# Optimization experiments

Measured on AMD Instinct MI355X. Metric: run time of the kernel, lower is better.

The kernel has to match this reference:

```python
import jax, jax.numpy as jnp
import numpy as np

N_ITEMS = 7000
N_USERS = 30000
N_NODES = N_ITEMS + N_USERS  # 37000
D = 128        # embed_dim == user_embed_dim
E = 400000     # num edges
R = 10         # n_relation (num ratings)
NB = 8         # num_bases
B = 512        # batch of conversations
L = 100        # max context items per sample


def setup_inputs() -> dict:
    key = jax.random.key(0)
    ks = jax.random.split(key, 16)
    # edges: item (source) -> user (target), disjoint id ranges as in load_data
    src = jax.random.randint(ks[0], (E,), 0, N_ITEMS)
    dst = jax.random.randint(ks[1], (E,), N_ITEMS, N_NODES)
    edge_index = jnp.stack([src, dst]).astype(jnp.int64)
    edge_type = jax.random.randint(ks[2], (E,), 0, R).astype(jnp.int64)

    def make_ctx(k1, k2):
        c = jax.random.randint(k1, (B, L), 0, N_ITEMS)
        drop = jax.random.uniform(k2, (B, L)) < 0.3  # -1 padding as in batch lists
        return jnp.where(drop, -1, c).astype(jnp.int64)

    ctx_init = make_ctx(ks[3], ks[4])
    ctx_resp = make_ctx(ks[5], ks[6])

    s = 0.02
    basis = jax.random.normal(ks[7], (NB, N_NODES, D), jnp.float32) * s
    comp = jax.random.normal(ks[8], (R, NB), jnp.float32) * s
    root = jax.random.normal(ks[9], (N_NODES, D), jnp.float32) * s
    bias = jnp.zeros((D,), jnp.float32)
    attn_a = jax.random.normal(ks[10], (D, D), jnp.float32) * s
    attn_b = jax.random.normal(ks[11], (D,), jnp.float32) * s
    fc1_w = jax.random.normal(ks[12], (D, D), jnp.float32) * s
    fc1_b = jnp.zeros((D,), jnp.float32)
    fc2_w = jax.random.normal(ks[13], (D, D), jnp.float32) * s
    fc2_b = jnp.zeros((D,), jnp.float32)
    efc1_w = jax.random.normal(ks[14], (2 * D, D), jnp.float32) * s
    efc1_b = jnp.zeros((D,), jnp.float32)
    efc2_w = jax.random.normal(ks[15], (D, D), jnp.float32) * s
    efc2_b = jnp.zeros((D,), jnp.float32)
    return dict(edge_index=edge_index, edge_type=edge_type, ctx_init=ctx_init,
                ctx_resp=ctx_resp, basis=basis, comp=comp, root=root, bias=bias,
                attn_a=attn_a, attn_b=attn_b, fc1_w=fc1_w, fc1_b=fc1_b,
                fc2_w=fc2_w, fc2_b=fc2_b, efc1_w=efc1_w, efc1_b=efc1_b,
                efc2_w=efc2_w, efc2_b=efc2_b)


def _rgcn(basis, comp, root, bias, edge_index, edge_type):
    # RGCNConv with x=None: per-edge message W_{r_e}[src_e], mean-aggregated
    # per (target, relation), summed over relations, plus root lookup + bias.
    src, dst = edge_index[0], edge_index[1]
    nb, n, d = basis.shape
    r = comp.shape[0]
    cpe = comp[edge_type]  # [E, NB]
    msg = jnp.zeros((src.shape[0], d), basis.dtype)
    for b in range(nb):  # small fixed basis count; avoids [E,NB,D] gather
        msg = msg + cpe[:, b:b + 1] * basis[b][src]
    seg = dst * r + edge_type  # per-(node, relation) segment for mean aggr
    sums = jax.ops.segment_sum(msg, seg, num_segments=n * r).reshape(n, r, d)
    cnt = jax.ops.segment_sum(jnp.ones_like(edge_type, basis.dtype), seg,
                              num_segments=n * r).reshape(n, r, 1)
    return root + bias + (sums / jnp.maximum(cnt, 1.0)).sum(axis=1)  # [N, D]


def _item_user_means(node_emb, edge_index):
    # mean over users connected to each item (edge_idx[1][edge_idx[0]==item])
    src, dst = edge_index[0], edge_index[1]
    isum = jax.ops.segment_sum(node_emb[dst], src, num_segments=N_ITEMS)
    icnt = jax.ops.segment_sum(jnp.ones_like(src, node_emb.dtype), src,
                               num_segments=N_ITEMS)
    item_mean = isum / jnp.maximum(icnt, 1.0)[:, None]  # [N_ITEMS, D]
    return item_mean, icnt > 0


def _attn_pool(ctx, item_mean, item_has_users, attn_a, attn_b):
    # SelfAttentionBatch over each sample's item reps (padding/-1 & degree-0
    # items masked out; all-empty samples -> zeros, as in original).
    valid = ctx >= 0
    idx = jnp.clip(ctx, 0, N_ITEMS - 1)
    h = item_mean[idx]                       # [B, L, D]
    valid = valid & item_has_users[idx]
    e = jnp.einsum('bld,d->bl', jnp.tanh(jnp.einsum('bld,de->ble', h, attn_a)),
                   attn_b)
    attn = jax.nn.softmax(jnp.where(valid, e, -1e9), axis=-1)
    attn = jnp.where(valid, attn, 0.0)
    return jnp.einsum('bl,bld->bd', attn, h)  # [B, D]


def _project(x, w1, b1, w2, b2):
    # fc1 -> relu -> fc2 -> relu (as in _project_user_interaction_*)
    return jax.nn.relu(jax.nn.relu(x @ w1 + b1) @ w2 + b2)


def reference(edge_index, edge_type, ctx_init, ctx_resp, basis, comp, root,
              bias, attn_a, attn_b, fc1_w, fc1_b, fc2_w, fc2_b, efc1_w,
              efc1_b, efc2_w, efc2_b):
    node_emb = _rgcn(basis, comp, root, bias, edge_index, edge_type)
    item_mean, item_has = _item_user_means(node_emb, edge_index)
    p_init = _project(_attn_pool(ctx_init, item_mean, item_has, attn_a, attn_b),
                      fc1_w, fc1_b, fc2_w, fc2_b)
    p_resp = _project(_attn_pool(ctx_resp, item_mean, item_has, attn_a, attn_b),
                      fc1_w, fc1_b, fc2_w, fc2_b)
    both = jnp.concatenate([p_init, p_resp], axis=1)  # [B, 2D]
    profile = _project(both, efc1_w, efc1_b, efc2_w, efc2_b)  # [B, D]
    return profile, p_init, p_resp
```

## Files before the change

kernel.cpp:

```cpp
#include <hip/hip_runtime.h>
#include <math.h>

typedef unsigned int uint;

#define N_ITEMS 7000
#define N_NODES 37000
#define N_USERS 30000
#define DIM     128
#define HD      64
#define NREL    10
#define NBASES  8
#define BATCH   512
#define CTXL    100
#define E_MAX   400000

#define UCAP    64
#define ICAP    128

#define OFF_CNT    0
#define OFF_ICNT   (OFF_CNT + N_USERS * NREL)
#define OFF_UCNT   (OFF_ICNT + N_ITEMS)
#define ZERO_ELEMS (OFF_UCNT + N_USERS)
#define OFF_ICSR   ZERO_ELEMS
#define OFF_UCSR   (OFF_ICSR + N_ITEMS * ICAP)
#define OFF_WC     (OFF_UCSR + N_USERS * UCAP)
#define OFF_ACC    (OFF_WC + NREL * N_ITEMS * HD)
#define OFF_MEAN   (OFF_ACC + N_USERS * HD)
#define OFF_SCORE  (OFF_MEAN + N_ITEMS * HD)

__device__ __forceinline__ float2 bf2f(uint p) {
  float2 r;
  r.x = __uint_as_float(p << 16);
  r.y = __uint_as_float(p & 0xffff0000u);
  return r;
}
__device__ __forceinline__ uint f2bf(float x, float y) {
  uint a = __float_as_uint(x), b = __float_as_uint(y);
  a += 0x7fffu + ((a >> 16) & 1u);
  b += 0x7fffu + ((b >> 16) & 1u);
  return (a >> 16) | (b & 0xffff0000u);
}

__device__ __forceinline__ float wave_sum(float v) {
#pragma unroll
  for (int o = 1; o < 64; o <<= 1) v += __shfl_xor(v, o, 64);
  return v;
}
__device__ __forceinline__ float wave_max(float v) {
#pragma unroll
  for (int o = 1; o < 64; o <<= 1) v = fmaxf(v, __shfl_xor(v, o, 64));
  return v;
}

#define COMBINE_BLOCKS (N_ITEMS / 4)
__global__ __launch_bounds__(256) void k_initfill(const float* __restrict__ basis,
                                                  const float* __restrict__ comp,
                                                  uint* __restrict__ Wc,
                                                  const int* __restrict__ ei,
                                                  const int* __restrict__ et, int E,
                                                  int* __restrict__ cnt,
                                                  int* __restrict__ icnt,
                                                  int* __restrict__ ucnt,
                                                  int* __restrict__ icsr,
                                                  int* __restrict__ ucsr) {
  int tid = threadIdx.x;
  if (blockIdx.x < COMBINE_BLOCKS) {
    int i = blockIdx.x * 4 + (tid >> 6);
    int lane = tid & 63;
    float2 bb[NBASES];
#pragma unroll
    for (int b = 0; b < NBASES; ++b)
      bb[b] = ((const float2*)basis)[((size_t)b * N_NODES + i) * HD + lane];
#pragma unroll
    for (int r = 0; r < NREL; ++r) {
      float sx = 0.f, sy = 0.f;
#pragma unroll
      for (int b = 0; b < NBASES; ++b) {
        float c = comp[r * NBASES + b];
        sx = fmaf(c, bb[b].x, sx);
        sy = fmaf(c, bb[b].y, sy);
      }
      Wc[((size_t)i * NREL + r) * HD + lane] = f2bf(sx, sy);
    }
  } else {
    int e = (blockIdx.x - COMBINE_BLOCKS) * 256 + tid;
    if (e < E) {
      int s  = ei[e];
      int u0 = ei[E + e] - N_ITEMS;
      int t  = et[e];
      atomicAdd(&cnt[u0 * NREL + t], 1);
      int si = atomicAdd(&icnt[s], 1);
      if (si < ICAP) icsr[s * ICAP + si] = u0;
      int su = atomicAdd(&ucnt[u0], 1);
      if (su < UCAP) ucsr[u0 * UCAP + su] = s | (t << 16);
    }
  }
}

__global__ __launch_bounds__(256) void k_useragg(const int* __restrict__ ucnt,
                                                 const int* __restrict__ ucsr,
                                                 const int* __restrict__ cnt,
                                                 const uint* __restrict__ Wc,
                                                 const float* __restrict__ root,
                                                 uint* __restrict__ acc) {
  int tid = threadIdx.x;
  int u = blockIdx.x * 4 + (tid >> 6);
  int lane = tid & 63;
  int deg = ucnt[u];
  if (deg > UCAP) deg = UCAP;
  int base = u * UCAP;
  float wl = 0.f;
  if (lane < NREL) {
    int c = cnt[u * NREL + lane];
    wl = (c > 0) ? 1.0f / (float)c : 0.0f;
  }
  float2 av[8];
#pragma unroll
  for (int k = 0; k < 8; ++k) { av[k].x = 0.f; av[k].y = 0.f; }
  for (int j0 = 0; j0 < deg; j0 += 64) {
    int m = deg - j0;
    if (m > 64) m = 64;
    int pl = (lane < m) ? ucsr[base + j0 + lane] : 0;
    for (int kk = 0; kk < m; kk += 16) {
#pragma unroll
      for (int k = 0; k < 16; ++k) {
        int idx = kk + k;
        int p = __shfl(pl, idx & 63);
        int r = p >> 16;
        float w = (idx < m) ? __shfl(wl, r) : 0.f;
        uint q = Wc[((size_t)(p & 0xffff) * NREL + r) * HD + lane];
        float2 f = bf2f(q);
        av[k & 7].x = fmaf(w, f.x, av[k & 7].x);
        av[k & 7].y = fmaf(w, f.y, av[k & 7].y);
      }
    }
  }
  float2 rt = ((const float2*)root)[(size_t)(N_ITEMS + u) * HD + lane];
  rt.x += ((av[0].x + av[1].x) + (av[2].x + av[3].x)) +
          ((av[4].x + av[5].x) + (av[6].x + av[7].x));
  rt.y += ((av[0].y + av[1].y) + (av[2].y + av[3].y)) +
          ((av[4].y + av[5].y) + (av[6].y + av[7].y));
  acc[(size_t)u * HD + lane] = f2bf(rt.x, rt.y);
}

__global__ __launch_bounds__(256) void k_itemagg(const int* __restrict__ icnt,
                                                 const int* __restrict__ icsr,
                                                 const uint* __restrict__ acc,
                                                 const float* __restrict__ bias,
                                                 const float* __restrict__ attn_a,
                                                 const float* __restrict__ attn_b,
                                                 uint* __restrict__ mean,
                                                 float* __restrict__ score) {
  int tid = threadIdx.x;
  int i = blockIdx.x * 4 + (tid >> 6);
  int lane = tid & 63;
  int deg = icnt[i];
  int degc = (deg > ICAP) ? ICAP : deg;
  int base = i * ICAP;
  float2 av[8];
#pragma unroll
  for (int k = 0; k < 8; ++k) { av[k].x = 0.f; av[k].y = 0.f; }
  for (int j0 = 0; j0 < degc; j0 += 64) {
    int m = degc - j0;
    if (m > 64) m = 64;
    int pl = (lane < m) ? icsr[base + j0 + lane] : 0;
    for (int kk = 0; kk < m; kk += 16) {
#pragma unroll
      for (int k = 0; k < 16; ++k) {
        int idx = kk + k;
        int u0 = __shfl(pl, idx & 63);
        uint q = acc[(size_t)u0 * HD + lane];
        float2 f = bf2f(q);
        if (idx < m) {
          av[k & 7].x += f.x;
          av[k & 7].y += f.y;
        }
      }
    }
  }
  float sx = ((av[0].x + av[1].x) + (av[2].x + av[3].x)) +
             ((av[4].x + av[5].x) + (av[6].x + av[7].x));
  float sy = ((av[0].y + av[1].y) + (av[2].y + av[3].y)) +
             ((av[4].y + av[5].y) + (av[6].y + av[7].y));
  float2 mv = {0.f, 0.f};
  if (deg > 0) {
    float inv = 1.0f / (float)deg;
    float2 bv = ((const float2*)bias)[lane];
    mv.x = sx * inv + bv.x;
    mv.y = sy * inv + bv.y;
  }
  mean[(size_t)i * HD + lane] = f2bf(mv.x, mv.y);

  float z0 = 0.f, z1 = 0.f;
#pragma unroll 8
  for (int k2 = 0; k2 < HD; ++k2) {
    float hx = __shfl(mv.x, k2);
    float hy = __shfl(mv.y, k2);
    float2 w0 = ((const float2*)attn_a)[(size_t)(2 * k2) * HD + lane];
    float2 w1 = ((const float2*)attn_a)[(size_t)(2 * k2 + 1) * HD + lane];
    z0 = fmaf(hx, w0.x, z0); z1 = fmaf(hx, w0.y, z1);
    z0 = fmaf(hy, w1.x, z0); z1 = fmaf(hy, w1.y, z1);
  }
  float2 ab = ((const float2*)attn_b)[lane];
  float v = wave_sum(tanhf(z0) * ab.x + tanhf(z1) * ab.y);
  if (lane == 0) score[i] = (deg > 0) ? v : -1e9f;
}

__global__ __launch_bounds__(128) void k_batch2(const int* __restrict__ ctx0,
                                                const int* __restrict__ ctx1,
                                                const uint* __restrict__ mean,
                                                const float* __restrict__ score,
                                                const float* __restrict__ fc1_w,
                                                const float* __restrict__ fc1_b,
                                                const float* __restrict__ fc2_w,
                                                const float* __restrict__ fc2_b,
                                                const float* __restrict__ efc1_w,
                                                const float* __restrict__ efc1_b,
                                                const float* __restrict__ efc2_w,
                                                const float* __restrict__ efc2_b,
                                                float* __restrict__ out) {
  __shared__ float2 shp[2][HD];
  int b = blockIdx.x;
  int wv = threadIdx.x >> 6;
  int lane = threadIdx.x & 63;
  float2* out2 = (float2*)out;

  const int* cx = (wv ? ctx1 : ctx0) + (size_t)b * CTXL;
  int id0 = cx[lane];
  float e0 = (id0 >= 0) ? score[id0] : -1e9f;
  int id1 = -1;
  float e1 = -3.0e38f;
  if (lane < CTXL - 64) {
    id1 = cx[64 + lane];
    e1 = (id1 >= 0) ? score[id1] : -1e9f;
  }
  float mx = wave_max(fmaxf(e0, e1));
  float x0 = expf(e0 - mx);
  float x1 = (lane < CTXL - 64) ? expf(e1 - mx) : 0.f;
  float inv = 1.0f / wave_sum(x0 + x1);
  float w0 = (id0 >= 0) ? x0 * inv : 0.f;
  float w1 = (id1 >= 0) ? x1 * inv : 0.f;
  int i0 = (id0 >= 0) ? id0 : 0;
  int i1 = (id1 >= 0) ? id1 : 0;

  float2 av[4];
#pragma unroll
  for (int k = 0; k < 4; ++k) { av[k].x = 0.f; av[k].y = 0.f; }
  for (int j = 0; j < 64; j += 4) {
#pragma unroll
    for (int k = 0; k < 4; ++k) {
      int ii = __shfl(i0, j + k);
      float ww = __shfl(w0, j + k);
      float2 f = bf2f(mean[(size_t)ii * HD + lane]);
      av[k].x = fmaf(ww, f.x, av[k].x);
      av[k].y = fmaf(ww, f.y, av[k].y);
    }
  }
  for (int j = 0; j < CTXL - 64; j += 4) {
#pragma unroll
    for (int k = 0; k < 4; ++k) {
      int ii = __shfl(i1, j + k);
      float ww = __shfl(w1, j + k);
      float2 f = bf2f(mean[(size_t)ii * HD + lane]);
      av[k].x = fmaf(ww, f.x, av[k].x);
      av[k].y = fmaf(ww, f.y, av[k].y);
    }
  }
  float2 pool;
  pool.x = (av[0].x + av[1].x) + (av[2].x + av[3].x);
  pool.y = (av[0].y + av[1].y) + (av[2].y + av[3].y);

  float2 z = ((const float2*)fc1_b)[lane];
#pragma unroll 8
  for (int k2 = 0; k2 < HD; ++k2) {
    float hx = __shfl(pool.x, k2);
    float hy = __shfl(pool.y, k2);
    float2 wa = ((const float2*)fc1_w)[(size_t)(2 * k2) * HD + lane];
    float2 wb = ((const float2*)fc1_w)[(size_t)(2 * k2 + 1) * HD + lane];
    z.x = fmaf(hx, wa.x, z.x); z.y = fmaf(hx, wa.y, z.y);
    z.x = fmaf(hy, wb.x, z.x); z.y = fmaf(hy, wb.y, z.y);
  }
  z.x = fmaxf(z.x, 0.f);
  z.y = fmaxf(z.y, 0.f);

  float2 z2 = ((const float2*)fc2_b)[lane];
#pragma unroll 8
  for (int k2 = 0; k2 < HD; ++k2) {
    float hx = __shfl(z.x, k2);
    float hy = __shfl(z.y, k2);
    float2 wa = ((const float2*)fc2_w)[(size_t)(2 * k2) * HD + lane];
    float2 wb = ((const float2*)fc2_w)[(size_t)(2 * k2 + 1) * HD + lane];
    z2.x = fmaf(hx, wa.x, z2.x); z2.y = fmaf(hx, wa.y, z2.y);
    z2.x = fmaf(hy, wb.x, z2.x); z2.y = fmaf(hy, wb.y, z2.y);
  }
  z2.x = fmaxf(z2.x, 0.f);
  z2.y = fmaxf(z2.y, 0.f);
  out2[((size_t)(1 + wv) * BATCH + b) * HD + lane] = z2;
  shp[wv][lane] = z2;
  __syncthreads();

  if (wv == 0) {
    float2 p0 = shp[0][lane];
    float2 p1 = shp[1][lane];
    float2 zz = ((const float2*)efc1_b)[lane];
#pragma unroll 8
    for (int k2 = 0; k2 < HD; ++k2) {
      float hx = __shfl(p0.x, k2);
      float hy = __shfl(p0.y, k2);
      float2 wa = ((const float2*)efc1_w)[(size_t)(2 * k2) * HD + lane];
      float2 wb = ((const float2*)efc1_w)[(size_t)(2 * k2 + 1) * HD + lane];
      zz.x = fmaf(hx, wa.x, zz.x); zz.y = fmaf(hx, wa.y, zz.y);
      zz.x = fmaf(hy, wb.x, zz.x); zz.y = fmaf(hy, wb.y, zz.y);
    }
#pragma unroll 8
    for (int k2 = 0; k2 < HD; ++k2) {
      float hx = __shfl(p1.x, k2);
      float hy = __shfl(p1.y, k2);
      float2 wa = ((const float2*)efc1_w)[(size_t)(DIM + 2 * k2) * HD + lane];
      float2 wb = ((const float2*)efc1_w)[(size_t)(DIM + 2 * k2 + 1) * HD + lane];
      zz.x = fmaf(hx, wa.x, zz.x); zz.y = fmaf(hx, wa.y, zz.y);
      zz.x = fmaf(hy, wb.x, zz.x); zz.y = fmaf(hy, wb.y, zz.y);
    }
    zz.x = fmaxf(zz.x, 0.f);
    zz.y = fmaxf(zz.y, 0.f);

    float2 zf = ((const float2*)efc2_b)[lane];
#pragma unroll 8
    for (int k2 = 0; k2 < HD; ++k2) {
      float hx = __shfl(zz.x, k2);
      float hy = __shfl(zz.y, k2);
      float2 wa = ((const float2*)efc2_w)[(size_t)(2 * k2) * HD + lane];
      float2 wb = ((const float2*)efc2_w)[(size_t)(2 * k2 + 1) * HD + lane];
      zf.x = fmaf(hx, wa.x, zf.x); zf.y = fmaf(hx, wa.y, zf.y);
      zf.x = fmaf(hy, wb.x, zf.x); zf.y = fmaf(hy, wb.y, zf.y);
    }
    zf.x = fmaxf(zf.x, 0.f);
    zf.y = fmaxf(zf.y, 0.f);
    out2[(size_t)b * HD + lane] = zf;
  }
}

extern "C" void kernel_launch(void* const* d_in, const int* in_sizes, int n_in,
                              void* d_out, int out_size, void* d_ws, size_t ws_size,
                              hipStream_t stream) {
  const int*   ei     = (const int*)d_in[0];
  const int*   et     = (const int*)d_in[1];
  const int*   ctx0   = (const int*)d_in[2];
  const int*   ctx1   = (const int*)d_in[3];
  const float* basis  = (const float*)d_in[4];
  const float* comp   = (const float*)d_in[5];
  const float* root   = (const float*)d_in[6];
  const float* bias   = (const float*)d_in[7];
  const float* attn_a = (const float*)d_in[8];
  const float* attn_b = (const float*)d_in[9];
  const float* fc1_w  = (const float*)d_in[10];
  const float* fc1_b  = (const float*)d_in[11];
  const float* fc2_w  = (const float*)d_in[12];
  const float* fc2_b  = (const float*)d_in[13];
  const float* efc1_w = (const float*)d_in[14];
  const float* efc1_b = (const float*)d_in[15];
  const float* efc2_w = (const float*)d_in[16];
  const float* efc2_b = (const float*)d_in[17];
  float* out = (float*)d_out;

  const int E = in_sizes[1];

  float* ws   = (float*)d_ws;
  int*  cnt   = (int*)(ws + OFF_CNT);
  int*  icnt  = (int*)(ws + OFF_ICNT);
  int*  ucnt  = (int*)(ws + OFF_UCNT);
  int*  icsr  = (int*)(ws + OFF_ICSR);
  int*  ucsr  = (int*)(ws + OFF_UCSR);
  uint* Wc    = (uint*)(ws + OFF_WC);
  uint* acc   = (uint*)(ws + OFF_ACC);
  uint* mean  = (uint*)(ws + OFF_MEAN);
  float* score = ws + OFF_SCORE;

  hipMemsetAsync(d_ws, 0, (size_t)ZERO_ELEMS * sizeof(float), stream);

  int countBlocks = (E + 255) / 256;
  k_initfill<<<COMBINE_BLOCKS + countBlocks, 256, 0, stream>>>(
      basis, comp, Wc, ei, et, E, cnt, icnt, ucnt, icsr, ucsr);
  k_useragg<<<N_USERS / 4, 256, 0, stream>>>(ucnt, ucsr, cnt, Wc, root, acc);
  k_itemagg<<<N_ITEMS / 4, 256, 0, stream>>>(icnt, icsr, acc, bias, attn_a,
                                             attn_b, mean, score);
  k_batch2<<<BATCH, 128, 0, stream>>>(ctx0, ctx1, mean, score, fc1_w, fc1_b,
                                      fc2_w, fc2_b, efc1_w, efc1_b, efc2_w,
                                      efc2_b, out);
}
```

Before: 394.9 us.

## Process two nodes per wave and batch gathers before accumulating

Each wave in the user and item aggregation kernels now handles two nodes instead of one. It issues 32 independent row gathers into register arrays before doing any accumulation, so more loads are in flight at once and gather latency is hidden better. Both kernels gain a launch-bounds minimum-occupancy hint, and the grids are halved to match. The cost is higher register pressure and wasted work whenever the two paired nodes have unequal degrees, since the loop runs to the larger degree.

Measured after the change: 387.4 us, median of 2. No clear change (-1.9%).

```diff
diff --git a/kernel.cpp b/kernel.cpp
--- a/kernel.cpp
+++ b/kernel.cpp
@@ -97,113 +97,178 @@
   }
 }
 
-__global__ __launch_bounds__(256) void k_useragg(const int* __restrict__ ucnt,
-                                                 const int* __restrict__ ucsr,
-                                                 const int* __restrict__ cnt,
-                                                 const uint* __restrict__ Wc,
-                                                 const float* __restrict__ root,
-                                                 uint* __restrict__ acc) {
+__global__ __launch_bounds__(256, 4) void k_useragg(const int* __restrict__ ucnt,
+                                                    const int* __restrict__ ucsr,
+                                                    const int* __restrict__ cnt,
+                                                    const uint* __restrict__ Wc,
+                                                    const float* __restrict__ root,
+                                                    uint* __restrict__ acc) {
   int tid = threadIdx.x;
-  int u = blockIdx.x * 4 + (tid >> 6);
-  int lane = tid & 63;
-  int deg = ucnt[u];
-  if (deg > UCAP) deg = UCAP;
-  int base = u * UCAP;
-  float wl = 0.f;
+  int wid = tid >> 6, lane = tid & 63;
+  int uA = blockIdx.x * 8 + wid * 2;
+  int uB = uA + 1;
+  int degA = ucnt[uA]; if (degA > UCAP) degA = UCAP;
+  int degB = ucnt[uB]; if (degB > UCAP) degB = UCAP;
+  float wlA = 0.f, wlB = 0.f;
   if (lane < NREL) {
-    int c = cnt[u * NREL + lane];
-    wl = (c > 0) ? 1.0f / (float)c : 0.0f;
-  }
-  float2 av[8];
-#pragma unroll
-  for (int k = 0; k < 8; ++k) { av[k].x = 0.f; av[k].y = 0.f; }
-  for (int j0 = 0; j0 < deg; j0 += 64) {
-    int m = deg - j0;
-    if (m > 64) m = 64;
-    int pl = (lane < m) ? ucsr[base + j0 + lane] : 0;
-    for (int kk = 0; kk < m; kk += 16) {
-#pragma unroll
-      for (int k = 0; k < 16; ++k) {
-        int idx = kk + k;
-        int p = __shfl(pl, idx & 63);
-        int r = p >> 16;
-        float w = (idx < m) ? __shfl(wl, r) : 0.f;
-        uint q = Wc[((size_t)(p & 0xffff) * NREL + r) * HD + lane];
-        float2 f = bf2f(q);
-        av[k & 7].x = fmaf(w, f.x, av[k & 7].x);
-        av[k & 7].y = fmaf(w, f.y, av[k & 7].y);
-      }
-    }
-  }
-  float2 rt = ((const float2*)root)[(size_t)(N_ITEMS + u) * HD + lane];
-  rt.x += ((av[0].x + av[1].x) + (av[2].x + av[3].x)) +
-          ((av[4].x + av[5].x) + (av[6].x + av[7].x));
-  rt.y += ((av[0].y + av[1].y) + (av[2].y + av[3].y)) +
-          ((av[4].y + av[5].y) + (av[6].y + av[7].y));
-  acc[(size_t)u * HD + lane] = f2bf(rt.x, rt.y);
-}
-
-__global__ __launch_bounds__(256) void k_itemagg(const int* __restrict__ icnt,
-                                                 const int* __restrict__ icsr,
-                                                 const uint* __restrict__ acc,
-                                                 const float* __restrict__ bias,
-                                                 const float* __restrict__ attn_a,
-                                                 const float* __restrict__ attn_b,
-                                                 uint* __restrict__ mean,
-                                                 float* __restrict__ score) {
+    int cA = cnt[uA * NREL + lane];
+    int cB = cnt[uB * NREL + lane];
+    wlA = (cA > 0) ? 1.0f / (float)cA : 0.0f;
+    wlB = (cB > 0) ? 1.0f / (float)cB : 0.0f;
+  }
+  int plA = ucsr[uA * UCAP + lane];
+  int plB = ucsr[uB * UCAP + lane];
+
+  float2 avA[4], avB[4];
+#pragma unroll
+  for (int k = 0; k < 4; ++k) {
+    avA[k].x = 0.f; avA[k].y = 0.f;
+    avB[k].x = 0.f; avB[k].y = 0.f;
+  }
+  int mmax = (degA > degB) ? degA : degB;
+#pragma unroll 1
+  for (int kk = 0; kk < mmax; kk += 16) {
+    uint qA[16], qB[16];
+#pragma unroll
+    for (int k = 0; k < 16; ++k) {
+      int idx = kk + k;
+      int p = (idx < degA) ? __shfl(plA, idx & 63) : 0;
+      qA[k] = Wc[((size_t)(p & 0xffff) * NREL + (p >> 16)) * HD + lane];
+    }
+#pragma unroll
+    for (int k = 0; k < 16; ++k) {
+      int idx = kk + k;
+      int p = (idx < degB) ? __shfl(plB, idx & 63) : 0;
+      qB[k] = Wc[((size_t)(p & 0xffff) * NREL + (p >> 16)) * HD + lane];
+    }
+#pragma unroll
+    for (int k = 0; k < 16; ++k) {
+      int idx = kk + k;
+      int p = __shfl(plA, idx & 63);
+      float w = (idx < degA) ? __shfl(wlA, p >> 16) : 0.f;
+      float2 f = bf2f(qA[k]);
+      avA[k & 3].x = fmaf(w, f.x, avA[k & 3].x);
+      avA[k & 3].y = fmaf(w, f.y, avA[k & 3].y);
+    }
+#pragma unroll
+    for (int k = 0; k < 16; ++k) {
+      int idx = kk + k;
+      int p = __shfl(plB, idx & 63);
+      float w = (idx < degB) ? __shfl(wlB, p >> 16) : 0.f;
+      float2 f = bf2f(qB[k]);
+      avB[k & 3].x = fmaf(w, f.x, avB[k & 3].x);
+      avB[k & 3].y = fmaf(w, f.y, avB[k & 3].y);
+    }
+  }
+  float2 rtA = ((const float2*)root)[(size_t)(N_ITEMS + uA) * HD + lane];
+  float2 rtB = ((const float2*)root)[(size_t)(N_ITEMS + uB) * HD + lane];
+  rtA.x += (avA[0].x + avA[1].x) + (avA[2].x + avA[3].x);
+  rtA.y += (avA[0].y + avA[1].y) + (avA[2].y + avA[3].y);
+  rtB.x += (avB[0].x + avB[1].x) + (avB[2].x + avB[3].x);
+  rtB.y += (avB[0].y + avB[1].y) + (avB[2].y + avB[3].y);
+  acc[(size_t)uA * HD + lane] = f2bf(rtA.x, rtA.y);
+  acc[(size_t)uB * HD + lane] = f2bf(rtB.x, rtB.y);
+}
+
+__global__ __launch_bounds__(256, 4) void k_itemagg(const int* __restrict__ icnt,
+                                                    const int* __restrict__ icsr,
+                                                    const uint* __restrict__ acc,
+                                                    const float* __restrict__ bias,
+                                                    const float* __restrict__ attn_a,
+                                                    const float* __restrict__ attn_b,
+                                                    uint* __restrict__ mean,
+                                                    float* __restrict__ score) {
   int tid = threadIdx.x;
-  int i = blockIdx.x * 4 + (tid >> 6);
-  int lane = tid & 63;
-  int deg = icnt[i];
-  int degc = (deg > ICAP) ? ICAP : deg;
-  int base = i * ICAP;
-  float2 av[8];
-#pragma unroll
-  for (int k = 0; k < 8; ++k) { av[k].x = 0.f; av[k].y = 0.f; }
-  for (int j0 = 0; j0 < degc; j0 += 64) {
-    int m = degc - j0;
-    if (m > 64) m = 64;
-    int pl = (lane < m) ? icsr[base + j0 + lane] : 0;
-    for (int kk = 0; kk < m; kk += 16) {
-#pragma unroll
-      for (int k = 0; k < 16; ++k) {
-        int idx = kk + k;
-        int u0 = __shfl(pl, idx & 63);
-        uint q = acc[(size_t)u0 * HD + lane];
-        float2 f = bf2f(q);
-        if (idx < m) {
-          av[k & 7].x += f.x;
-          av[k & 7].y += f.y;
-        }
-      }
-    }
-  }
-  float sx = ((av[0].x + av[1].x) + (av[2].x + av[3].x)) +
-             ((av[4].x + av[5].x) + (av[6].x + av[7].x));
-  float sy = ((av[0].y + av[1].y) + (av[2].y + av[3].y)) +
-             ((av[4].y + av[5].y) + (av[6].y + av[7].y));
-  float2 mv = {0.f, 0.f};
-  if (deg > 0) {
-    float inv = 1.0f / (float)deg;
-    float2 bv = ((const float2*)bias)[lane];
-    mv.x = sx * inv + bv.x;
-    mv.y = sy * inv + bv.y;
-  }
-  mean[(size_t)i * HD + lane] = f2bf(mv.x, mv.y);
-
-  float z0 = 0.f, z1 = 0.f;
+  int wid = tid >> 6, lane = tid & 63;
+  int iA = blockIdx.x * 8 + wid * 2;
+  int iB = iA + 1;
+  int degA = icnt[iA], degB = icnt[iB];
+  int dcA = (degA > ICAP) ? ICAP : degA;
+  int dcB = (degB > ICAP) ? ICAP : degB;
+  int plA0 = icsr[iA * ICAP + lane];
+  int plA1 = icsr[iA * ICAP + 64 + lane];
+  int plB0 = icsr[iB * ICAP + lane];
+  int plB1 = icsr[iB * ICAP + 64 + lane];
+
+  float2 avA[4], avB[4];
+#pragma unroll
+  for (int k = 0; k < 4; ++k) {
+    avA[k].x = 0.f; avA[k].y = 0.f;
+    avB[k].x = 0.f; avB[k].y = 0.f;
+  }
+  int mmax = (dcA > dcB) ? dcA : dcB;
+#pragma unroll 1
+  for (int kk = 0; kk < mmax; kk += 16) {
+    int plAc = (kk < 64) ? plA0 : plA1;
+    int plBc = (kk < 64) ? plB0 : plB1;
+    uint qA[16], qB[16];
+#pragma unroll
+    for (int k = 0; k < 16; ++k) {
+      int idx = kk + k;
+      int u0 = (idx < dcA) ? __shfl(plAc, idx & 63) : 0;
+      qA[k] = acc[(size_t)u0 * HD + lane];
+    }
+#pragma unroll
+    for (int k = 0; k < 16; ++k) {
+      int idx = kk + k;
+      int u0 = (idx < dcB) ? __shfl(plBc, idx & 63) : 0;
+      qB[k] = acc[(size_t)u0 * HD + lane];
+    }
+#pragma unroll
+    for (int k = 0; k < 16; ++k) {
+      int idx = kk + k;
+      float w = (idx < dcA) ? 1.0f : 0.0f;
+      float2 f = bf2f(qA[k]);
+      avA[k & 3].x = fmaf(w, f.x, avA[k & 3].x);
+      avA[k & 3].y = fmaf(w, f.y, avA[k & 3].y);
+    }
+#pragma unroll
+    for (int k = 0; k < 16; ++k) {
+      int idx = kk + k;
+      float w = (idx < dcB) ? 1.0f : 0.0f;
+      float2 f = bf2f(qB[k]);
+      avB[k & 3].x = fmaf(w, f.x, avB[k & 3].x);
+      avB[k & 3].y = fmaf(w, f.y, avB[k & 3].y);
+    }
+  }
+  float sxA = (avA[0].x + avA[1].x) + (avA[2].x + avA[3].x);
+  float syA = (avA[0].y + avA[1].y) + (avA[2].y + avA[3].y);
+  float sxB = (avB[0].x + avB[1].x) + (avB[2].x + avB[3].x);
+  float syB = (avB[0].y + avB[1].y) + (avB[2].y + avB[3].y);
+  float2 bv = ((const float2*)bias)[lane];
+  float2 mvA = {0.f, 0.f}, mvB = {0.f, 0.f};
+  if (degA > 0) {
+    float inv = 1.0f / (float)degA;
+    mvA.x = sxA * inv + bv.x;
+    mvA.y = syA * inv + bv.y;
+  }
+  if (degB > 0) {
+    float inv = 1.0f / (float)degB;
+    mvB.x = sxB * inv + bv.x;
+    mvB.y = syB * inv + bv.y;
+  }
+  mean[(size_t)iA * HD + lane] = f2bf(mvA.x, mvA.y);
+  mean[(size_t)iB * HD + lane] = f2bf(mvB.x, mvB.y);
+
+  float z0A = 0.f, z1A = 0.f, z0B = 0.f, z1B = 0.f;
 #pragma unroll 8
   for (int k2 = 0; k2 < HD; ++k2) {
-    float hx = __shfl(mv.x, k2);
-    float hy = __shfl(mv.y, k2);
     float2 w0 = ((const float2*)attn_a)[(size_t)(2 * k2) * HD + lane];
     float2 w1 = ((const float2*)attn_a)[(size_t)(2 * k2 + 1) * HD + lane];
-    z0 = fmaf(hx, w0.x, z0); z1 = fmaf(hx, w0.y, z1);
-    z0 = fmaf(hy, w1.x, z0); z1 = fmaf(hy, w1.y, z1);
+    float hxA = __shfl(mvA.x, k2), hyA = __shfl(mvA.y, k2);
+    float hxB = __shfl(mvB.x, k2), hyB = __shfl(mvB.y, k2);
+    z0A = fmaf(hxA, w0.x, z0A); z1A = fmaf(hxA, w0.y, z1A);
+    z0A = fmaf(hyA, w1.x, z0A); z1A = fmaf(hyA, w1.y, z1A);
+    z0B = fmaf(hxB, w0.x, z0B); z1B = fmaf(hxB, w0.y, z1B);
+    z0B = fmaf(hyB, w1.x, z0B); z1B = fmaf(hyB, w1.y, z1B);
   }
   float2 ab = ((const float2*)attn_b)[lane];
-  float v = wave_sum(tanhf(z0) * ab.x + tanhf(z1) * ab.y);
-  if (lane == 0) score[i] = (deg > 0) ? v : -1e9f;
+  float vA = wave_sum(tanhf(z0A) * ab.x + tanhf(z1A) * ab.y);
+  float vB = wave_sum(tanhf(z0B) * ab.x + tanhf(z1B) * ab.y);
+  if (lane == 0) {
+    score[iA] = (degA > 0) ? vA : -1e9f;
+    score[iB] = (degB > 0) ? vB : -1e9f;
+  }
 }
 
 __global__ __launch_bounds__(128) void k_batch2(const int* __restrict__ ctx0,
@@ -381,8 +446,8 @@
   int countBlocks = (E + 255) / 256;
   k_initfill<<<COMBINE_BLOCKS + countBlocks, 256, 0, stream>>>(
       basis, comp, Wc, ei, et, E, cnt, icnt, ucnt, icsr, ucsr);
-  k_useragg<<<N_USERS / 4, 256, 0, stream>>>(ucnt, ucsr, cnt, Wc, root, acc);
-  k_itemagg<<<N_ITEMS / 4, 256, 0, stream>>>(icnt, icsr, acc, bias, attn_a,
+  k_useragg<<<N_USERS / 8, 256, 0, stream>>>(ucnt, ucsr, cnt, Wc, root, acc);
+  k_itemagg<<<N_ITEMS / 8, 256, 0, stream>>>(icnt, icsr, acc, bias, attn_a,
                                              attn_b, mean, score);
   k_batch2<<<BATCH, 128, 0, stream>>>(ctx0, ctx1, mean, score, fc1_w, fc1_b,
                                       fc2_w, fc2_b, efc1_w, efc1_b, efc2_w,
```

## Batch four nodes per wave in aggregation and derive relation counts via ballot

Applied to the files above, without the earlier changes.

Removes the per-(user,relation) atomic count array and instead computes per-relation degree counts inside the user aggregation kernel using wave ballots over the user's edge list. User and item aggregation kernels now process four nodes per wave, issuing all gathers for a 16-edge chunk before accumulating to raise memory-level parallelism. The item attention matvec reuses each attn_a load across the four nodes. k_batch2 packs two samples per 256-thread block. The trade-offs are higher register pressure and idle lanes when degrees differ across the four grouped nodes.

Measured after the change: 393.7 us. About the same (-0.3%).

```diff
diff --git a/kernel.cpp b/kernel.cpp
--- a/kernel.cpp
+++ b/kernel.cpp
@@ -17,8 +17,7 @@
 #define UCAP    64
 #define ICAP    128
 
-#define OFF_CNT    0
-#define OFF_ICNT   (OFF_CNT + N_USERS * NREL)
+#define OFF_ICNT   0
 #define OFF_UCNT   (OFF_ICNT + N_ITEMS)
 #define ZERO_ELEMS (OFF_UCNT + N_USERS)
 #define OFF_ICSR   ZERO_ELEMS
@@ -58,7 +57,6 @@
                                                   uint* __restrict__ Wc,
                                                   const int* __restrict__ ei,
                                                   const int* __restrict__ et, int E,
-                                                  int* __restrict__ cnt,
                                                   int* __restrict__ icnt,
                                                   int* __restrict__ ucnt,
                                                   int* __restrict__ icsr,
@@ -88,7 +86,6 @@
       int s  = ei[e];
       int u0 = ei[E + e] - N_ITEMS;
       int t  = et[e];
-      atomicAdd(&cnt[u0 * NREL + t], 1);
       int si = atomicAdd(&icnt[s], 1);
       if (si < ICAP) icsr[s * ICAP + si] = u0;
       int su = atomicAdd(&ucnt[u0], 1);
@@ -97,116 +94,190 @@
   }
 }
 
-__global__ __launch_bounds__(256) void k_useragg(const int* __restrict__ ucnt,
-                                                 const int* __restrict__ ucsr,
-                                                 const int* __restrict__ cnt,
-                                                 const uint* __restrict__ Wc,
-                                                 const float* __restrict__ root,
-                                                 uint* __restrict__ acc) {
+__global__ __launch_bounds__(256, 3) void k_useragg(const int* __restrict__ ucnt,
+                                                    const int* __restrict__ ucsr,
+                                                    const uint* __restrict__ Wc,
+                                                    const float* __restrict__ root,
+                                                    uint* __restrict__ acc) {
   int tid = threadIdx.x;
-  int u = blockIdx.x * 4 + (tid >> 6);
-  int lane = tid & 63;
-  int deg = ucnt[u];
-  if (deg > UCAP) deg = UCAP;
-  int base = u * UCAP;
-  float wl = 0.f;
-  if (lane < NREL) {
-    int c = cnt[u * NREL + lane];
-    wl = (c > 0) ? 1.0f / (float)c : 0.0f;
-  }
-  float2 av[8];
-#pragma unroll
-  for (int k = 0; k < 8; ++k) { av[k].x = 0.f; av[k].y = 0.f; }
-  for (int j0 = 0; j0 < deg; j0 += 64) {
-    int m = deg - j0;
-    if (m > 64) m = 64;
-    int pl = (lane < m) ? ucsr[base + j0 + lane] : 0;
-    for (int kk = 0; kk < m; kk += 16) {
-#pragma unroll
-      for (int k = 0; k < 16; ++k) {
-        int idx = kk + k;
-        int p = __shfl(pl, idx & 63);
-        int r = p >> 16;
-        float w = (idx < m) ? __shfl(wl, r) : 0.f;
-        uint q = Wc[((size_t)(p & 0xffff) * NREL + r) * HD + lane];
-        float2 f = bf2f(q);
-        av[k & 7].x = fmaf(w, f.x, av[k & 7].x);
-        av[k & 7].y = fmaf(w, f.y, av[k & 7].y);
-      }
-    }
-  }
-  float2 rt = ((const float2*)root)[(size_t)(N_ITEMS + u) * HD + lane];
-  rt.x += ((av[0].x + av[1].x) + (av[2].x + av[3].x)) +
-          ((av[4].x + av[5].x) + (av[6].x + av[7].x));
-  rt.y += ((av[0].y + av[1].y) + (av[2].y + av[3].y)) +
-          ((av[4].y + av[5].y) + (av[6].y + av[7].y));
-  acc[(size_t)u * HD + lane] = f2bf(rt.x, rt.y);
-}
-
-__global__ __launch_bounds__(256) void k_itemagg(const int* __restrict__ icnt,
-                                                 const int* __restrict__ icsr,
-                                                 const uint* __restrict__ acc,
-                                                 const float* __restrict__ bias,
-                                                 const float* __restrict__ attn_a,
-                                                 const float* __restrict__ attn_b,
-                                                 uint* __restrict__ mean,
-                                                 float* __restrict__ score) {
+  int wid = tid >> 6, lane = tid & 63;
+  int u0i = blockIdx.x * 16 + wid * 4;
+
+  int deg[4], pl[4];
+  float wl[4];
+#pragma unroll
+  for (int n = 0; n < 4; ++n) {
+    int u = u0i + n;
+    int d = ucnt[u];
+    deg[n] = (d > UCAP) ? UCAP : d;
+    pl[n] = ucsr[u * UCAP + lane];
+    wl[n] = 0.f;
+  }
+  {
+    bool v[4];
+    int rr[4];
+#pragma unroll
+    for (int n = 0; n < 4; ++n) { v[n] = lane < deg[n]; rr[n] = pl[n] >> 16; }
+#pragma unroll
+    for (int r = 0; r < NREL; ++r) {
+#pragma unroll
+      for (int n = 0; n < 4; ++n) {
+        float c = (float)__popcll(__ballot(v[n] && (rr[n] == r)));
+        if (lane == r) wl[n] = (c > 0.f) ? 1.0f / c : 0.0f;
+      }
+    }
+  }
+
+  float2 av[4][4];
+#pragma unroll
+  for (int n = 0; n < 4; ++n)
+#pragma unroll
+    for (int k = 0; k < 4; ++k) { av[n][k].x = 0.f; av[n][k].y = 0.f; }
+
+  int mmax = deg[0];
+#pragma unroll
+  for (int n = 1; n < 4; ++n) if (deg[n] > mmax) mmax = deg[n];
+
+#pragma unroll 1
+  for (int kk = 0; kk < mmax; kk += 16) {
+    uint q[4][16];
+#pragma unroll
+    for (int n = 0; n < 4; ++n) {
+      if (kk < deg[n]) {
+#pragma unroll
+        for (int k = 0; k < 16; ++k) {
+          int idx = kk + k;
+          int p = (idx < deg[n]) ? __shfl(pl[n], idx & 63) : 0;
+          q[n][k] = Wc[((size_t)(p & 0xffff) * NREL + (p >> 16)) * HD + lane];
+        }
+      }
+    }
+#pragma unroll
+    for (int n = 0; n < 4; ++n) {
+      if (kk < deg[n]) {
+#pragma unroll
+        for (int k = 0; k < 16; ++k) {
+          int idx = kk + k;
+          int p = __shfl(pl[n], idx & 63);
+          float w = (idx < deg[n]) ? __shfl(wl[n], p >> 16) : 0.f;
+          float2 f = bf2f(q[n][k]);
+          av[n][k & 3].x = fmaf(w, f.x, av[n][k & 3].x);
+          av[n][k & 3].y = fmaf(w, f.y, av[n][k & 3].y);
+        }
+      }
+    }
+  }
+#pragma unroll
+  for (int n = 0; n < 4; ++n) {
+    int u = u0i + n;
+    float2 rt = ((const float2*)root)[(size_t)(N_ITEMS + u) * HD + lane];
+    rt.x += (av[n][0].x + av[n][1].x) + (av[n][2].x + av[n][3].x);
+    rt.y += (av[n][0].y + av[n][1].y) + (av[n][2].y + av[n][3].y);
+    acc[(size_t)u * HD + lane] = f2bf(rt.x, rt.y);
+  }
+}
+
+__global__ __launch_bounds__(256, 3) void k_itemagg(const int* __restrict__ icnt,
+                                                    const int* __restrict__ icsr,
+                                                    const uint* __restrict__ acc,
+                                                    const float* __restrict__ bias,
+                                                    const float* __restrict__ attn_a,
+                                                    const float* __restrict__ attn_b,
+                                                    uint* __restrict__ mean,
+                                                    float* __restrict__ score) {
   int tid = threadIdx.x;
-  int i = blockIdx.x * 4 + (tid >> 6);
-  int lane = tid & 63;
-  int deg = icnt[i];
-  int degc = (deg > ICAP) ? ICAP : deg;
-  int base = i * ICAP;
-  float2 av[8];
-#pragma unroll
-  for (int k = 0; k < 8; ++k) { av[k].x = 0.f; av[k].y = 0.f; }
-  for (int j0 = 0; j0 < degc; j0 += 64) {
-    int m = degc - j0;
-    if (m > 64) m = 64;
-    int pl = (lane < m) ? icsr[base + j0 + lane] : 0;
-    for (int kk = 0; kk < m; kk += 16) {
-#pragma unroll
-      for (int k = 0; k < 16; ++k) {
-        int idx = kk + k;
-        int u0 = __shfl(pl, idx & 63);
-        uint q = acc[(size_t)u0 * HD + lane];
-        float2 f = bf2f(q);
-        if (idx < m) {
-          av[k & 7].x += f.x;
-          av[k & 7].y += f.y;
+  int wid = tid >> 6, lane = tid & 63;
+  int i0 = blockIdx.x * 16 + wid * 4;
+
+  int degr[4], dc[4], pl0[4], pl1[4], ia[4];
+  bool vn[4];
+#pragma unroll
+  for (int n = 0; n < 4; ++n) {
+    int i = i0 + n;
+    vn[n] = i < N_ITEMS;
+    ia[n] = vn[n] ? i : 0;
+    degr[n] = vn[n] ? icnt[ia[n]] : 0;
+    dc[n] = (degr[n] > ICAP) ? ICAP : degr[n];
+    pl0[n] = icsr[ia[n] * ICAP + lane];
+    pl1[n] = icsr[ia[n] * ICAP + 64 + lane];
+  }
+
+  float2 av[4][4];
+#pragma unroll
+  for (int n = 0; n < 4; ++n)
+#pragma unroll
+    for (int k = 0; k < 4; ++k) { av[n][k].x = 0.f; av[n][k].y = 0.f; }
+
+  int mmax = dc[0];
+#pragma unroll
+  for (int n = 1; n < 4; ++n) if (dc[n] > mmax) mmax = dc[n];
+
+#pragma unroll 1
+  for (int kk = 0; kk < mmax; kk += 16) {
+    uint q[4][16];
+#pragma unroll
+    for (int n = 0; n < 4; ++n) {
+      if (kk < dc[n]) {
+        int plc = (kk < 64) ? pl0[n] : pl1[n];
+#pragma unroll
+        for (int k = 0; k < 16; ++k) {
+          int idx = kk + k;
+          int u0 = (idx < dc[n]) ? __shfl(plc, idx & 63) : 0;
+          q[n][k] = acc[(size_t)u0 * HD + lane];
         }
       }
     }
-  }
-  float sx = ((av[0].x + av[1].x) + (av[2].x + av[3].x)) +
-             ((av[4].x + av[5].x) + (av[6].x + av[7].x));
-  float sy = ((av[0].y + av[1].y) + (av[2].y + av[3].y)) +
-             ((av[4].y + av[5].y) + (av[6].y + av[7].y));
-  float2 mv = {0.f, 0.f};
-  if (deg > 0) {
-    float inv = 1.0f / (float)deg;
-    float2 bv = ((const float2*)bias)[lane];
-    mv.x = sx * inv + bv.x;
-    mv.y = sy * inv + bv.y;
-  }
-  mean[(size_t)i * HD + lane] = f2bf(mv.x, mv.y);
-
-  float z0 = 0.f, z1 = 0.f;
-#pragma unroll 8
+#pragma unroll
+    for (int n = 0; n < 4; ++n) {
+      if (kk < dc[n]) {
+#pragma unroll
+        for (int k = 0; k < 16; ++k) {
+          int idx = kk + k;
+          float w = (idx < dc[n]) ? 1.0f : 0.0f;
+          float2 f = bf2f(q[n][k]);
+          av[n][k & 3].x = fmaf(w, f.x, av[n][k & 3].x);
+          av[n][k & 3].y = fmaf(w, f.y, av[n][k & 3].y);
+        }
+      }
+    }
+  }
+
+  float2 bv = ((const float2*)bias)[lane];
+  float2 mv[4];
+#pragma unroll
+  for (int n = 0; n < 4; ++n) {
+    float sx = (av[n][0].x + av[n][1].x) + (av[n][2].x + av[n][3].x);
+    float sy = (av[n][0].y + av[n][1].y) + (av[n][2].y + av[n][3].y);
+    mv[n].x = 0.f; mv[n].y = 0.f;
+    if (degr[n] > 0) {
+      float inv = 1.0f / (float)degr[n];
+      mv[n].x = sx * inv + bv.x;
+      mv[n].y = sy * inv + bv.y;
+    }
+    if (vn[n]) mean[(size_t)ia[n] * HD + lane] = f2bf(mv[n].x, mv[n].y);
+  }
+
+  float z0[4] = {0.f, 0.f, 0.f, 0.f}, z1[4] = {0.f, 0.f, 0.f, 0.f};
+#pragma unroll 4
   for (int k2 = 0; k2 < HD; ++k2) {
-    float hx = __shfl(mv.x, k2);
-    float hy = __shfl(mv.y, k2);
     float2 w0 = ((const float2*)attn_a)[(size_t)(2 * k2) * HD + lane];
     float2 w1 = ((const float2*)attn_a)[(size_t)(2 * k2 + 1) * HD + lane];
-    z0 = fmaf(hx, w0.x, z0); z1 = fmaf(hx, w0.y, z1);
-    z0 = fmaf(hy, w1.x, z0); z1 = fmaf(hy, w1.y, z1);
+#pragma unroll
+    for (int n = 0; n < 4; ++n) {
+      float hx = __shfl(mv[n].x, k2), hy = __shfl(mv[n].y, k2);
+      z0[n] = fmaf(hx, w0.x, z0[n]); z1[n] = fmaf(hx, w0.y, z1[n]);
+      z0[n] = fmaf(hy, w1.x, z0[n]); z1[n] = fmaf(hy, w1.y, z1[n]);
+    }
   }
   float2 ab = ((const float2*)attn_b)[lane];
-  float v = wave_sum(tanhf(z0) * ab.x + tanhf(z1) * ab.y);
-  if (lane == 0) score[i] = (deg > 0) ? v : -1e9f;
-}
-
-__global__ __launch_bounds__(128) void k_batch2(const int* __restrict__ ctx0,
+#pragma unroll
+  for (int n = 0; n < 4; ++n) {
+    float v = wave_sum(tanhf(z0[n]) * ab.x + tanhf(z1[n]) * ab.y);
+    if (lane == 0 && vn[n]) score[ia[n]] = (degr[n] > 0) ? v : -1e9f;
+  }
+}
+
+__global__ __launch_bounds__(256) void k_batch2(const int* __restrict__ ctx0,
                                                 const int* __restrict__ ctx1,
                                                 const uint* __restrict__ mean,
                                                 const float* __restrict__ score,
@@ -219,13 +290,15 @@
                                                 const float* __restrict__ efc2_w,
                                                 const float* __restrict__ efc2_b,
                                                 float* __restrict__ out) {
-  __shared__ float2 shp[2][HD];
-  int b = blockIdx.x;
-  int wv = threadIdx.x >> 6;
+  __shared__ float2 shp[2][2][HD];
+  int wid = threadIdx.x >> 6;
   int lane = threadIdx.x & 63;
+  const int pairIdx = wid >> 1;
+  const int side    = wid & 1;
+  int b = blockIdx.x * 2 + pairIdx;
   float2* out2 = (float2*)out;
 
-  const int* cx = (wv ? ctx1 : ctx0) + (size_t)b * CTXL;
+  const int* cx = (side ? ctx1 : ctx0) + (size_t)b * CTXL;
   int id0 = cx[lane];
   float e0 = (id0 >= 0) ? score[id0] : -1e9f;
   int id1 = -1;
@@ -295,13 +368,13 @@
   }
   z2.x = fmaxf(z2.x, 0.f);
   z2.y = fmaxf(z2.y, 0.f);
-  out2[((size_t)(1 + wv) * BATCH + b) * HD + lane] = z2;
-  shp[wv][lane] = z2;
+  out2[((size_t)(1 + side) * BATCH + b) * HD + lane] = z2;
+  shp[pairIdx][side][lane] = z2;
   __syncthreads();
 
-  if (wv == 0) {
-    float2 p0 = shp[0][lane];
-    float2 p1 = shp[1][lane];
+  if (side == 0) {
+    float2 p0 = shp[pairIdx][0][lane];
+    float2 p1 = shp[pairIdx][1][lane];
     float2 zz = ((const float2*)efc1_b)[lane];
 #pragma unroll 8
     for (int k2 = 0; k2 < HD; ++k2) {
@@ -366,7 +439,6 @@
   const int E = in_sizes[1];
 
   float* ws   = (float*)d_ws;
-  int*  cnt   = (int*)(ws + OFF_CNT);
   int*  icnt  = (int*)(ws + OFF_ICNT);
   int*  ucnt  = (int*)(ws + OFF_UCNT);
   int*  icsr  = (int*)(ws + OFF_ICSR);
@@ -380,11 +452,11 @@
 
   int countBlocks = (E + 255) / 256;
   k_initfill<<<COMBINE_BLOCKS + countBlocks, 256, 0, stream>>>(
-      basis, comp, Wc, ei, et, E, cnt, icnt, ucnt, icsr, ucsr);
-  k_useragg<<<N_USERS / 4, 256, 0, stream>>>(ucnt, ucsr, cnt, Wc, root, acc);
-  k_itemagg<<<N_ITEMS / 4, 256, 0, stream>>>(icnt, icsr, acc, bias, attn_a,
-                                             attn_b, mean, score);
-  k_batch2<<<BATCH, 128, 0, stream>>>(ctx0, ctx1, mean, score, fc1_w, fc1_b,
-                                      fc2_w, fc2_b, efc1_w, efc1_b, efc2_w,
-                                      efc2_b, out);
-}
+      basis, comp, Wc, ei, et, E, icnt, ucnt, icsr, ucsr);
+  k_useragg<<<N_USERS / 16, 256, 0, stream>>>(ucnt, ucsr, Wc, root, acc);
+  k_itemagg<<<(N_ITEMS + 15) / 16, 256, 0, stream>>>(icnt, icsr, acc, bias,
+                                                     attn_a, attn_b, mean, score);
+  k_batch2<<<BATCH / 2, 256, 0, stream>>>(ctx0, ctx1, mean, score, fc1_w, fc1_b,
+                                          fc2_w, fc2_b, efc1_w, efc1_b, efc2_w,
+                                          efc2_b, out);
+}
```
